# Kernel optimization log

Hardware: AMD Instinct MI355X
Metric: run time of the kernel (lower is better)

The kernel has to match this reference:

```python
import jax, jax.numpy as jnp
import numpy as np

EPS = 1e-5

def _ln(x, g, b):
    m = x.mean(-1, keepdims=True)
    v = ((x - m) ** 2).mean(-1, keepdims=True)
    return (x - m) * jax.lax.rsqrt(v + EPS) * g + b

def _glu(z):
    a, g = jnp.split(z, 2, axis=-1)
    return a * jax.nn.sigmoid(g)

def setup_inputs() -> dict:
    key = jax.random.key(0)
    ks = jax.random.split(key, 8)
    B, T, V, I, H = 64, 512, 32, 64, 64
    s = 0.02
    return {
        "x": jax.random.normal(ks[0], (B, T, V, I), dtype=jnp.float32),
        # weight GRN: (V*I) -> V
        "wg_W1": jax.random.normal(ks[1], (V * I, V), dtype=jnp.float32) * s,
        "wg_b1": jnp.zeros((V,), jnp.float32),
        "wg_W2": jax.random.normal(ks[2], (V, V), dtype=jnp.float32) * s,
        "wg_b2": jnp.zeros((V,), jnp.float32),
        "wg_Wg": jax.random.normal(ks[3], (V, 2 * V), dtype=jnp.float32) * s,
        "wg_bg": jnp.zeros((2 * V,), jnp.float32),
        "wg_Ws": jax.random.normal(ks[4], (V * I, V), dtype=jnp.float32) * s,
        "wg_bs": jnp.zeros((V,), jnp.float32),
        "wg_gamma": jnp.ones((V,), jnp.float32),
        "wg_beta": jnp.zeros((V,), jnp.float32),
        # per-variable GRNs, batched over V: I -> H (I == H, skip is identity)
        "v_W1": jax.random.normal(ks[5], (V, I, H), dtype=jnp.float32) * s,
        "v_b1": jnp.zeros((V, H), jnp.float32),
        "v_W2": jax.random.normal(ks[6], (V, H, H), dtype=jnp.float32) * s,
        "v_b2": jnp.zeros((V, H), jnp.float32),
        "v_Wg": jax.random.normal(ks[7], (V, H, 2 * H), dtype=jnp.float32) * s,
        "v_bg": jnp.zeros((V, 2 * H), jnp.float32),
        "v_gamma": jnp.ones((V, H), jnp.float32),
        "v_beta": jnp.zeros((V, H), jnp.float32),
    }

def reference(x, wg_W1, wg_b1, wg_W2, wg_b2, wg_Wg, wg_bg, wg_Ws, wg_bs,
              wg_gamma, wg_beta, v_W1, v_b1, v_W2, v_b2, v_Wg, v_bg,
              v_gamma, v_beta):
    B, T, V, I = x.shape
    # ---- variable-selection weights GRN on flattened input ----
    flat = x.reshape(B, T, V * I)                       # [B,T,V*I]
    skip = flat @ wg_Ws + wg_bs                          # [B,T,V] (proj skip: sizes differ)
    h = jax.nn.elu(flat @ wg_W1 + wg_b1)
    h = h @ wg_W2 + wg_b2
    w = _ln(skip + _glu(h @ wg_Wg + wg_bg), wg_gamma, wg_beta)
    w = jax.nn.softmax(w, axis=-1)                       # [B,T,V]
    # ---- per-variable GRNs, batched over V (skip = x since I == H) ----
    h = jax.nn.elu(jnp.einsum('btvi,vih->btvh', x, v_W1) + v_b1)
    h = jnp.einsum('btvh,vhk->btvk', h, v_W2) + v_b2
    g = jnp.einsum('btvh,vhk->btvk', h, v_Wg) + v_bg     # [B,T,V,2H]
    pv = _ln(x + _glu(g), v_gamma, v_beta)               # [B,T,V,H]
    # ---- softmax-weighted combination over variables ----
    return jnp.einsum('btv,btvh->bth', w, pv)            # [B,T,H]
```

## Files before the change

### kernel.cpp

```cpp
#include <hip/hip_runtime.h>

#define NT   32768
#define NV   32
#define DI   64
#define VI   2048

typedef __attribute__((ext_vector_type(8)))  short short8;
typedef __attribute__((ext_vector_type(16))) float floatx16;

#define MFMA32(a,b,c) __builtin_amdgcn_mfma_f32_32x32x16_bf16(a, b, c, 0, 0, 0)

#define WS_S      0
#define WS_WBUF   8388608
#define WS_WCOMBT 12582912
#define WS_WAV    12845056

static __device__ __forceinline__ unsigned short f2bf(float f) {
    union { float f; unsigned u; } v; v.f = f;
    unsigned r = v.u + 0x7FFFu + ((v.u >> 16) & 1u);
    return (unsigned short)(r >> 16);
}
static __device__ __forceinline__ unsigned pk2bf(float lo, float hi) {
    return (unsigned)f2bf(lo) | ((unsigned)f2bf(hi) << 16);
}
static __device__ __forceinline__ float elu1(float v) {
    return (v > 0.f) ? v : (__expf(v) - 1.f);
}

__global__ void k0_prep(const float* __restrict__ wg_W1, const float* __restrict__ wg_Ws,
                        const float* __restrict__ v_W1, const float* __restrict__ v_b1,
                        const float* __restrict__ v_W2, const float* __restrict__ v_b2,
                        const float* __restrict__ v_Wg, const float* __restrict__ v_bg,
                        unsigned short* __restrict__ WcombT, unsigned short* __restrict__ wAv) {
    int tid = blockIdx.x * blockDim.x + threadIdx.x;
    int stride = gridDim.x * blockDim.x;
    for (int i = tid; i < 64 * 2048; i += stride) {
        int n = i >> 11, k = i & 2047;
        float val = (n < 32) ? wg_Ws[k * 32 + n] : wg_W1[k * 32 + (n - 32)];
        WcombT[i] = f2bf(val);
    }
    for (int i = tid; i < 32 * 256 * 88; i += stride) {
        int v  = i / (256 * 88);
        int rm = i - v * (256 * 88);
        int r  = rm / 88, c = rm - r * 88;
        float val = 0.f;
        if (r < 64) {
            if (c < 64)       val = v_W1[(v * 64 + c) * 64 + r];
            else if (c == 64) val = v_b1[v * 64 + r];
        } else if (r < 128) {
            int m = r - 64;
            if (c < 64)       val = v_W2[(v * 64 + c) * 64 + m];
            else if (c == 64) val = v_b2[v * 64 + m];
        } else {
            int m = r - 128;
            if (c < 64)       val = v_Wg[(v * 64 + c) * 128 + m];
            else if (c == 64) val = v_bg[v * 128 + m];
        }
        wAv[i] = f2bf(val);
    }
}

__launch_bounds__(256, 4)
__global__ void k1_wgemm(const float* __restrict__ x, const unsigned short* __restrict__ WcombT,
                         const float* __restrict__ wg_bs, const float* __restrict__ wg_b1,
                         float* __restrict__ S) {
    __shared__ float Cbuf[4 * 64 * 33];
    int tid  = threadIdx.x;
    int wv   = tid >> 6;
    int lane = tid & 63;
    int l31  = lane & 31, s = lane >> 5;
    int tile = blockIdx.x;
    long tok = (long)tile * 32 + l31;

    const float*          xrow = x + tok * VI + wv * 512 + s * 8;
    const unsigned short* a0p  = WcombT + (l31)      * 2048 + wv * 512 + s * 8;
    const unsigned short* a1p  = WcombT + (l31 + 32) * 2048 + wv * 512 + s * 8;

    floatx16 acc0 = {}; floatx16 acc1 = {};
    #pragma unroll 4
    for (int ks = 0; ks < 32; ++ks) {
        int ko = ks * 16;
        short8 af0 = *(const short8*)(a0p + ko);
        short8 af1 = *(const short8*)(a1p + ko);
        float4 xa = *(const float4*)(xrow + ko);
        float4 xb = *(const float4*)(xrow + ko + 4);
        union { unsigned u[4]; short8 s8; } bp;
        bp.u[0] = pk2bf(xa.x, xa.y);
        bp.u[1] = pk2bf(xa.z, xa.w);
        bp.u[2] = pk2bf(xb.x, xb.y);
        bp.u[3] = pk2bf(xb.z, xb.w);
        acc0 = MFMA32(af0, bp.s8, acc0);
        acc1 = MFMA32(af1, bp.s8, acc1);
    }
    float* cb = Cbuf + wv * (64 * 33);
    #pragma unroll
    for (int reg = 0; reg < 16; ++reg) {
        int r0 = (reg & 3) + 8 * (reg >> 2) + 4 * s;
        cb[(r0)*33 + l31]      = acc0[reg];
        cb[(r0 + 32)*33 + l31] = acc1[reg];
    }
    __syncthreads();
    int n  = tid & 63;
    int tb = (tid >> 6) * 8;
    #pragma unroll
    for (int g = 0; g < 8; ++g) {
        int t = tb + g;
        float v = Cbuf[0*2112 + n*33 + t] + Cbuf[1*2112 + n*33 + t]
                + Cbuf[2*2112 + n*33 + t] + Cbuf[3*2112 + n*33 + t];
        if (n < 32) v += wg_bs[n];
        else        v = elu1(v + wg_b1[n - 32]);
        S[((long)tile * 32 + t) * 64 + n] = v;
    }
}

__launch_bounds__(256, 4)
__global__ void k2_token(const float* __restrict__ S,
                         const float* __restrict__ wg_W2, const float* __restrict__ wg_b2,
                         const float* __restrict__ wg_Wg, const float* __restrict__ wg_bg,
                         const float* __restrict__ wg_gamma, const float* __restrict__ wg_beta,
                         float* __restrict__ wout) {
    int tid = threadIdx.x;
    int wv = tid >> 6, lane = tid & 63;
    int l31 = lane & 31;
    long t = (long)blockIdx.x * 4 + wv;
    float sv = S[t * 64 + lane];
    float h2 = wg_b2[l31];
    #pragma unroll
    for (int k = 0; k < 32; ++k) {
        float h1e = __shfl(sv, 32 + k);
        h2 += h1e * wg_W2[k * 32 + l31];
    }
    float z = wg_bg[lane];
    #pragma unroll
    for (int k = 0; k < 32; ++k) {
        float hk = __shfl(h2, k);
        z += hk * wg_Wg[k * 64 + lane];
    }
    float za   = __shfl(z, l31);
    float zg   = __shfl(z, l31 + 32);
    float skip = __shfl(sv, l31);
    float y = skip + za / (1.f + __expf(-zg));
    float s1 = y;
    #pragma unroll
    for (int m = 1; m <= 16; m <<= 1) s1 += __shfl_xor(s1, m);
    float mean = s1 * (1.f / 32.f);
    float d = y - mean;
    float s2 = d * d;
    #pragma unroll
    for (int m = 1; m <= 16; m <<= 1) s2 += __shfl_xor(s2, m);
    float rinv  = rsqrtf(s2 * (1.f / 32.f) + 1e-5f);
    float logit = d * rinv * wg_gamma[l31] + wg_beta[l31];
    float mx = logit;
    #pragma unroll
    for (int m = 1; m <= 16; m <<= 1) mx = fmaxf(mx, __shfl_xor(mx, m));
    float e = __expf(logit - mx);
    float se = e;
    #pragma unroll
    for (int m = 1; m <= 16; m <<= 1) se += __shfl_xor(se, m);
    if (lane < 32) wout[t * 32 + lane] = e / se;
}

static __device__ __forceinline__ void tile_to_bfrags(const float* t16, int sh,
                                                      short8* f0, short8* f1) {
    unsigned P[8];
    #pragma unroll
    for (int i = 0; i < 8; ++i) P[i] = pk2bf(t16[2 * i], t16[2 * i + 1]);
    unsigned X[8];
    #pragma unroll
    for (int i = 0; i < 8; ++i) X[i] = (unsigned)__shfl_xor((int)P[i], 32);
    union { unsigned u[4]; short8 s8; } a, b;
    a.u[0] = sh ? X[2] : P[0];  a.u[1] = sh ? X[3] : P[1];
    a.u[2] = sh ? P[2] : X[0];  a.u[3] = sh ? P[3] : X[1];
    b.u[0] = sh ? X[6] : P[4];  b.u[1] = sh ? X[7] : P[5];
    b.u[2] = sh ? P[6] : X[4];  b.u[3] = sh ? P[7] : X[5];
    *f0 = a.s8; *f1 = b.s8;
}

__launch_bounds__(256, 2)
__global__ void k3_vgrn(const float* __restrict__ x, const unsigned short* __restrict__ wAv,
                        const float* __restrict__ v_gamma, const float* __restrict__ v_beta,
                        const float* __restrict__ wbuf, float* __restrict__ out) {
    __shared__ float xt[128 * 65];
    __shared__ __align__(16) unsigned short wA[256 * 88];
    __shared__ float gb[128];
    int tid  = threadIdx.x;
    int wv   = tid >> 6, lane = tid & 63;
    int l31  = lane & 31, s = lane >> 5;
    int tile = blockIdx.x >> 1;
    int vh   = blockIdx.x & 1;
    int tl   = wv * 32 + l31;
    long tokg = (long)tile * 128 + tl;

    float outacc[32];
    #pragma unroll
    for (int i = 0; i < 32; ++i) outacc[i] = 0.f;

    union { unsigned u[4]; short8 s8; } onef;
    onef.u[0] = (s == 0) ? 0x00003F80u : 0u;
    onef.u[1] = 0; onef.u[2] = 0; onef.u[3] = 0;

    const unsigned short* wArow = wA + l31 * 88 + s * 8;

    for (int it = 0; it < 16; ++it) {
        int vg = vh * 16 + it;
        __syncthreads();
        {
            const float* xsrc = x + ((long)tile * 128 * NV + vg) * DI;
            #pragma unroll
            for (int i2 = 0; i2 < 8; ++i2) {
                int idx = i2 * 256 + tid;
                int row = idx >> 4, c4 = (idx & 15) * 4;
                float4 val = *(const float4*)(xsrc + (long)row * VI + c4);
                float* dst = xt + row * 65 + c4;
                dst[0] = val.x; dst[1] = val.y; dst[2] = val.z; dst[3] = val.w;
            }
        }
        {
            const uint4* wsrc = (const uint4*)(wAv + (long)vg * 256 * 88);
            uint4* wdst = (uint4*)wA;
            #pragma unroll
            for (int i2 = 0; i2 < 11; ++i2) {
                int c = i2 * 256 + tid;
                wdst[c] = wsrc[c];
            }
        }
        if (tid < 128) {
            int h = tid >> 1;
            gb[tid] = (tid & 1) ? v_beta[vg * 64 + h] : v_gamma[vg * 64 + h];
        }
        __syncthreads();

        short8 xb[4];
        const float* xr = xt + tl * 65 + s * 8;
        #pragma unroll
        for (int ks = 0; ks < 4; ++ks) {
            const float* p = xr + ks * 16;
            union { unsigned u[4]; short8 s8; } bp;
            bp.u[0] = pk2bf(p[0], p[1]);
            bp.u[1] = pk2bf(p[2], p[3]);
            bp.u[2] = pk2bf(p[4], p[5]);
            bp.u[3] = pk2bf(p[6], p[7]);
            xb[ks] = bp.s8;
        }
        floatx16 h1a0 = {}, h1a1 = {};
        #pragma unroll
        for (int ks = 0; ks < 5; ++ks) {
            short8 b = (ks < 4) ? xb[ks] : onef.s8;
            h1a0 = MFMA32(*(const short8*)(wArow + (0)   * 88 + ks * 16), b, h1a0);
            h1a1 = MFMA32(*(const short8*)(wArow + (32)  * 88 + ks * 16), b, h1a1);
        }
        short8 h1b[4];
        {
            float t16[16];
            #pragma unroll
            for (int r = 0; r < 16; ++r) t16[r] = elu1(h1a0[r]);
            tile_to_bfrags(t16, s, &h1b[0], &h1b[1]);
            #pragma unroll
            for (int r = 0; r < 16; ++r) t16[r] = elu1(h1a1[r]);
            tile_to_bfrags(t16, s, &h1b[2], &h1b[3]);
        }
        floatx16 h2a0 = {}, h2a1 = {};
        #pragma unroll
        for (int ks = 0; ks < 5; ++ks) {
            short8 b = (ks < 4) ? h1b[ks] : onef.s8;
            h2a0 = MFMA32(*(const short8*)(wArow + (64)  * 88 + ks * 16), b, h2a0);
            h2a1 = MFMA32(*(const short8*)(wArow + (96)  * 88 + ks * 16), b, h2a1);
        }
        short8 h2b[4];
        {
            float t16[16];
            #pragma unroll
            for (int r = 0; r < 16; ++r) t16[r] = h2a0[r];
            tile_to_bfrags(t16, s, &h2b[0], &h2b[1]);
            #pragma unroll
            for (int r = 0; r < 16; ++r) t16[r] = h2a1[r];
            tile_to_bfrags(t16, s, &h2b[2], &h2b[3]);
        }
        floatx16 g0 = {}, g1 = {}, g2 = {}, g3 = {};
        #pragma unroll
        for (int ks = 0; ks < 5; ++ks) {
            short8 b = (ks < 4) ? h2b[ks] : onef.s8;
            g0 = MFMA32(*(const short8*)(wArow + (128) * 88 + ks * 16), b, g0);
            g1 = MFMA32(*(const short8*)(wArow + (160) * 88 + ks * 16), b, g1);
            g2 = MFMA32(*(const short8*)(wArow + (192) * 88 + ks * 16), b, g2);
            g3 = MFMA32(*(const short8*)(wArow + (224) * 88 + ks * 16), b, g3);
        }
        float y[32];
        #pragma unroll
        for (int r = 0; r < 16; ++r) {
            int hr = (r & 3) + 8 * (r >> 2) + 4 * s;
            float glu0 = g0[r] / (1.f + __expf(-g2[r]));
            float glu1 = g1[r] / (1.f + __expf(-g3[r]));
            y[r]      = xt[tl * 65 + hr]      + glu0;
            y[16 + r] = xt[tl * 65 + 32 + hr] + glu1;
        }
        float s1 = 0.f;
        #pragma unroll
        for (int i = 0; i < 32; ++i) s1 += y[i];
        s1 += __shfl_xor(s1, 32);
        float mean = s1 * (1.f / 64.f);
        float s2 = 0.f;
        #pragma unroll
        for (int i = 0; i < 32; ++i) { float d = y[i] - mean; s2 += d * d; }
        s2 += __shfl_xor(s2, 32);
        float rinv = rsqrtf(s2 * (1.f / 64.f) + 1e-5f);
        float wvv = wbuf[tokg * 32 + vg];
        #pragma unroll
        for (int r = 0; r < 16; ++r) {
            int hr = (r & 3) + 8 * (r >> 2) + 4 * s;
            float pv0 = (y[r]      - mean) * rinv * gb[2*hr]        + gb[2*hr + 1];
            float pv1 = (y[16 + r] - mean) * rinv * gb[2*(hr+32)]   + gb[2*(hr+32) + 1];
            outacc[r]      += wvv * pv0;
            outacc[16 + r] += wvv * pv1;
        }
    }
    #pragma unroll
    for (int r = 0; r < 16; ++r) {
        int hr = (r & 3) + 8 * (r >> 2) + 4 * s;
        atomicAdd(out + tokg * 64 + hr,      outacc[r]);
        atomicAdd(out + tokg * 64 + 32 + hr, outacc[16 + r]);
    }
}

extern "C" void kernel_launch(void* const* d_in, const int* in_sizes, int n_in,
                              void* d_out, int out_size, void* d_ws, size_t ws_size,
                              hipStream_t stream) {
    const float* x        = (const float*)d_in[0];
    const float* wg_W1    = (const float*)d_in[1];
    const float* wg_b1    = (const float*)d_in[2];
    const float* wg_W2    = (const float*)d_in[3];
    const float* wg_b2    = (const float*)d_in[4];
    const float* wg_Wg    = (const float*)d_in[5];
    const float* wg_bg    = (const float*)d_in[6];
    const float* wg_Ws    = (const float*)d_in[7];
    const float* wg_bs    = (const float*)d_in[8];
    const float* wg_gamma = (const float*)d_in[9];
    const float* wg_beta  = (const float*)d_in[10];
    const float* v_W1     = (const float*)d_in[11];
    const float* v_b1     = (const float*)d_in[12];
    const float* v_W2     = (const float*)d_in[13];
    const float* v_b2     = (const float*)d_in[14];
    const float* v_Wg     = (const float*)d_in[15];
    const float* v_bg     = (const float*)d_in[16];
    const float* v_gamma  = (const float*)d_in[17];
    const float* v_beta   = (const float*)d_in[18];
    (void)in_sizes; (void)n_in; (void)ws_size;

    char* ws = (char*)d_ws;
    float* S               = (float*)(ws + WS_S);
    float* wbuf            = (float*)(ws + WS_WBUF);
    unsigned short* WcombT = (unsigned short*)(ws + WS_WCOMBT);
    unsigned short* wAv    = (unsigned short*)(ws + WS_WAV);
    float* out             = (float*)d_out;

    hipMemsetAsync(d_out, 0, (size_t)out_size * sizeof(float), stream);
    k0_prep<<<512, 256, 0, stream>>>(wg_W1, wg_Ws, v_W1, v_b1, v_W2, v_b2, v_Wg, v_bg,
                                     WcombT, wAv);
    k1_wgemm<<<1024, 256, 0, stream>>>(x, WcombT, wg_bs, wg_b1, S);
    k2_token<<<8192, 256, 0, stream>>>(S, wg_W2, wg_b2, wg_Wg, wg_bg, wg_gamma, wg_beta, wbuf);
    k3_vgrn<<<512, 256, 0, stream>>>(x, wAv, v_gamma, v_beta, wbuf, out);
}
```

Before: 675.2 us.

## Fold W2 into gate weights and restructure per-variable GRN kernel

Since there is no nonlinearity between the second linear layer and the gate projection, the prep kernel now precomputes W2·Wg (plus the folded biases) for both the weight GRN and the per-variable GRNs. This removes one matmul stage per token in k2 and one MFMA stage in k3. k3 also stages x in shared memory as bf16, reuses those bf16 fragments via cross-lane shuffles for the residual, shrinks LDS so three blocks fit per CU, and splits variables into 4 groups of 8 over 1024 blocks, which doubles the number of atomic adds to the output. The folded product is computed in fp32 and then rounded to bf16, and the residual now uses bf16 x instead of fp32, which slightly changes numerics.

```diff
diff --git a/kernel.cpp b/kernel.cpp
--- a/kernel.cpp
+++ b/kernel.cpp
@@ -14,6 +14,8 @@
 #define WS_WBUF   8388608
 #define WS_WCOMBT 12582912
 #define WS_WAV    12845056
+#define WS_WC2    13926400
+#define WS_BC2    13934592
 
 static __device__ __forceinline__ unsigned short f2bf(float f) {
     union { float f; unsigned u; } v; v.f = f;
@@ -26,37 +28,68 @@
 static __device__ __forceinline__ float elu1(float v) {
     return (v > 0.f) ? v : (__expf(v) - 1.f);
 }
+static __device__ __forceinline__ float bflo(unsigned v) {
+    union { unsigned u; float f; } t; t.u = v << 16; return t.f;
+}
+static __device__ __forceinline__ float bfhi(unsigned v) {
+    union { unsigned u; float f; } t; t.u = v & 0xFFFF0000u; return t.f;
+}
 
 __global__ void k0_prep(const float* __restrict__ wg_W1, const float* __restrict__ wg_Ws,
+                        const float* __restrict__ wg_W2, const float* __restrict__ wg_b2,
+                        const float* __restrict__ wg_Wg, const float* __restrict__ wg_bg,
                         const float* __restrict__ v_W1, const float* __restrict__ v_b1,
                         const float* __restrict__ v_W2, const float* __restrict__ v_b2,
                         const float* __restrict__ v_Wg, const float* __restrict__ v_bg,
-                        unsigned short* __restrict__ WcombT, unsigned short* __restrict__ wAv) {
+                        unsigned short* __restrict__ WcombT, unsigned short* __restrict__ wAv,
+                        float* __restrict__ Wc2, float* __restrict__ bc2) {
     int tid = blockIdx.x * blockDim.x + threadIdx.x;
-    int stride = gridDim.x * blockDim.x;
-    for (int i = tid; i < 64 * 2048; i += stride) {
+    int np  = gridDim.x * blockDim.x;
+    for (int i = tid; i < 64 * 2048; i += np) {
         int n = i >> 11, k = i & 2047;
         float val = (n < 32) ? wg_Ws[k * 32 + n] : wg_W1[k * 32 + (n - 32)];
         WcombT[i] = f2bf(val);
     }
-    for (int i = tid; i < 32 * 256 * 88; i += stride) {
-        int v  = i / (256 * 88);
-        int rm = i - v * (256 * 88);
-        int r  = rm / 88, c = rm - r * 88;
+    for (int i = tid; i < 32 * 64 * 88; i += np) {
+        int v  = i / (64 * 88);
+        int rm = i - v * (64 * 88);
+        int h  = rm / 88, c = rm - h * 88;
         float val = 0.f;
-        if (r < 64) {
-            if (c < 64)       val = v_W1[(v * 64 + c) * 64 + r];
-            else if (c == 64) val = v_b1[v * 64 + r];
-        } else if (r < 128) {
-            int m = r - 64;
-            if (c < 64)       val = v_W2[(v * 64 + c) * 64 + m];
-            else if (c == 64) val = v_b2[v * 64 + m];
+        if (c < 64)       val = v_W1[(v * 64 + c) * 64 + h];
+        else if (c == 64) val = v_b1[v * 64 + h];
+        wAv[v * 16896 + h * 88 + c] = f2bf(val);
+    }
+    for (int i = tid; i < 32 * 128 * 88; i += np) {
+        int v  = i / (128 * 88);
+        int rm = i - v * (128 * 88);
+        int n  = rm / 88, c = rm - n * 88;
+        float acc = 0.f;
+        if (c < 64) {
+            #pragma unroll 8
+            for (int k = 0; k < 64; ++k)
+                acc += v_W2[(v * 64 + c) * 64 + k] * v_Wg[(v * 64 + k) * 128 + n];
+        } else if (c == 64) {
+            #pragma unroll 8
+            for (int k = 0; k < 64; ++k)
+                acc += v_b2[v * 64 + k] * v_Wg[(v * 64 + k) * 128 + n];
+            acc += v_bg[v * 128 + n];
+        }
+        wAv[v * 16896 + (64 + n) * 88 + c] = f2bf(acc);
+    }
+    for (int i = tid; i < 32 * 64 + 64; i += np) {
+        if (i < 2048) {
+            int j = i >> 6, n = i & 63;
+            float acc = 0.f;
+            #pragma unroll 8
+            for (int k = 0; k < 32; ++k) acc += wg_W2[j * 32 + k] * wg_Wg[k * 64 + n];
+            Wc2[i] = acc;
         } else {
-            int m = r - 128;
-            if (c < 64)       val = v_Wg[(v * 64 + c) * 128 + m];
-            else if (c == 64) val = v_bg[v * 128 + m];
-        }
-        wAv[i] = f2bf(val);
+            int n = i - 2048;
+            float acc = 0.f;
+            #pragma unroll 8
+            for (int k = 0; k < 32; ++k) acc += wg_b2[k] * wg_Wg[k * 64 + n];
+            bc2[n] = acc + wg_bg[n];
+        }
     }
 }
 
@@ -115,8 +148,7 @@
 
 __launch_bounds__(256, 4)
 __global__ void k2_token(const float* __restrict__ S,
-                         const float* __restrict__ wg_W2, const float* __restrict__ wg_b2,
-                         const float* __restrict__ wg_Wg, const float* __restrict__ wg_bg,
+                         const float* __restrict__ Wc2, const float* __restrict__ bc2,
                          const float* __restrict__ wg_gamma, const float* __restrict__ wg_beta,
                          float* __restrict__ wout) {
     int tid = threadIdx.x;
@@ -124,17 +156,11 @@
     int l31 = lane & 31;
     long t = (long)blockIdx.x * 4 + wv;
     float sv = S[t * 64 + lane];
-    float h2 = wg_b2[l31];
+    float z = bc2[lane];
     #pragma unroll
     for (int k = 0; k < 32; ++k) {
-        float h1e = __shfl(sv, 32 + k);
-        h2 += h1e * wg_W2[k * 32 + l31];
-    }
-    float z = wg_bg[lane];
-    #pragma unroll
-    for (int k = 0; k < 32; ++k) {
-        float hk = __shfl(h2, k);
-        z += hk * wg_Wg[k * 64 + lane];
+        float hk = __shfl(sv, 32 + k);
+        z += hk * Wc2[k * 64 + lane];
     }
     float za   = __shfl(z, l31);
     float zg   = __shfl(z, l31 + 32);
@@ -176,20 +202,20 @@
     *f0 = a.s8; *f1 = b.s8;
 }
 
-__launch_bounds__(256, 2)
+__launch_bounds__(256, 3)
 __global__ void k3_vgrn(const float* __restrict__ x, const unsigned short* __restrict__ wAv,
                         const float* __restrict__ v_gamma, const float* __restrict__ v_beta,
                         const float* __restrict__ wbuf, float* __restrict__ out) {
-    __shared__ float xt[128 * 65];
-    __shared__ __align__(16) unsigned short wA[256 * 88];
+    __shared__ __align__(16) unsigned short wA[192 * 88];
+    __shared__ __align__(16) unsigned short xt[128 * 72];
     __shared__ float gb[128];
     int tid  = threadIdx.x;
     int wv   = tid >> 6, lane = tid & 63;
     int l31  = lane & 31, s = lane >> 5;
-    int tile = blockIdx.x >> 1;
-    int vh   = blockIdx.x & 1;
+    int vg   = blockIdx.x & 3;
+    int tb   = blockIdx.x >> 2;
     int tl   = wv * 32 + l31;
-    long tokg = (long)tile * 128 + tl;
+    long tokg = (long)tb * 128 + tl;
 
     float outacc[32];
     #pragma unroll
@@ -200,54 +226,46 @@
     onef.u[1] = 0; onef.u[2] = 0; onef.u[3] = 0;
 
     const unsigned short* wArow = wA + l31 * 88 + s * 8;
-
-    for (int it = 0; it < 16; ++it) {
-        int vg = vh * 16 + it;
+    int srow = tid >> 1, shalf = tid & 1;
+
+    for (int j8 = 0; j8 < 8; ++j8) {
+        int v = vg * 8 + j8;
         __syncthreads();
         {
-            const float* xsrc = x + ((long)tile * 128 * NV + vg) * DI;
+            const uint4* src = (const uint4*)(wAv + (long)v * 16896);
+            uint4* dst = (uint4*)wA;
+            for (int c = tid; c < 2112; c += 256) dst[c] = src[c];
+        }
+        {
+            const float* xs = x + ((long)tb * 128 + srow) * VI + v * 64 + shalf * 32;
+            unsigned short* xd = xt + srow * 72 + shalf * 32;
             #pragma unroll
-            for (int i2 = 0; i2 < 8; ++i2) {
-                int idx = i2 * 256 + tid;
-                int row = idx >> 4, c4 = (idx & 15) * 4;
-                float4 val = *(const float4*)(xsrc + (long)row * VI + c4);
-                float* dst = xt + row * 65 + c4;
-                dst[0] = val.x; dst[1] = val.y; dst[2] = val.z; dst[3] = val.w;
-            }
-        }
-        {
-            const uint4* wsrc = (const uint4*)(wAv + (long)vg * 256 * 88);
-            uint4* wdst = (uint4*)wA;
-            #pragma unroll
-            for (int i2 = 0; i2 < 11; ++i2) {
-                int c = i2 * 256 + tid;
-                wdst[c] = wsrc[c];
+            for (int q = 0; q < 4; ++q) {
+                float4 a = ((const float4*)xs)[2 * q];
+                float4 b = ((const float4*)xs)[2 * q + 1];
+                uint4 w;
+                w.x = pk2bf(a.x, a.y); w.y = pk2bf(a.z, a.w);
+                w.z = pk2bf(b.x, b.y); w.w = pk2bf(b.z, b.w);
+                ((uint4*)xd)[q] = w;
             }
         }
         if (tid < 128) {
             int h = tid >> 1;
-            gb[tid] = (tid & 1) ? v_beta[vg * 64 + h] : v_gamma[vg * 64 + h];
+            gb[tid] = (tid & 1) ? v_beta[v * 64 + h] : v_gamma[v * 64 + h];
         }
         __syncthreads();
 
-        short8 xb[4];
-        const float* xr = xt + tl * 65 + s * 8;
-        #pragma unroll
-        for (int ks = 0; ks < 4; ++ks) {
-            const float* p = xr + ks * 16;
-            union { unsigned u[4]; short8 s8; } bp;
-            bp.u[0] = pk2bf(p[0], p[1]);
-            bp.u[1] = pk2bf(p[2], p[3]);
-            bp.u[2] = pk2bf(p[4], p[5]);
-            bp.u[3] = pk2bf(p[6], p[7]);
-            xb[ks] = bp.s8;
-        }
+        union { short8 s8; unsigned u[4]; } xb[4];
+        #pragma unroll
+        for (int ks = 0; ks < 4; ++ks)
+            xb[ks].s8 = *(const short8*)(xt + tl * 72 + ks * 16 + s * 8);
+
         floatx16 h1a0 = {}, h1a1 = {};
         #pragma unroll
         for (int ks = 0; ks < 5; ++ks) {
-            short8 b = (ks < 4) ? xb[ks] : onef.s8;
-            h1a0 = MFMA32(*(const short8*)(wArow + (0)   * 88 + ks * 16), b, h1a0);
-            h1a1 = MFMA32(*(const short8*)(wArow + (32)  * 88 + ks * 16), b, h1a1);
+            short8 b = (ks < 4) ? xb[ks].s8 : onef.s8;
+            h1a0 = MFMA32(*(const short8*)(wArow + 0    + ks * 16), b, h1a0);
+            h1a1 = MFMA32(*(const short8*)(wArow + 2816 + ks * 16), b, h1a1);
         }
         short8 h1b[4];
         {
@@ -259,40 +277,38 @@
             for (int r = 0; r < 16; ++r) t16[r] = elu1(h1a1[r]);
             tile_to_bfrags(t16, s, &h1b[2], &h1b[3]);
         }
-        floatx16 h2a0 = {}, h2a1 = {};
+        floatx16 g0 = {}, g1 = {}, g2 = {}, g3 = {};
         #pragma unroll
         for (int ks = 0; ks < 5; ++ks) {
             short8 b = (ks < 4) ? h1b[ks] : onef.s8;
-            h2a0 = MFMA32(*(const short8*)(wArow + (64)  * 88 + ks * 16), b, h2a0);
-            h2a1 = MFMA32(*(const short8*)(wArow + (96)  * 88 + ks * 16), b, h2a1);
-        }
-        short8 h2b[4];
-        {
-            float t16[16];
+            g0 = MFMA32(*(const short8*)(wArow + 2 * 2816 + ks * 16), b, g0);
+            g1 = MFMA32(*(const short8*)(wArow + 3 * 2816 + ks * 16), b, g1);
+            g2 = MFMA32(*(const short8*)(wArow + 4 * 2816 + ks * 16), b, g2);
+            g3 = MFMA32(*(const short8*)(wArow + 5 * 2816 + ks * 16), b, g3);
+        }
+        unsigned ownu[4][2], Xu[4][2];
+        #pragma unroll
+        for (int kk = 0; kk < 4; ++kk) {
             #pragma unroll
-            for (int r = 0; r < 16; ++r) t16[r] = h2a0[r];
-            tile_to_bfrags(t16, s, &h2b[0], &h2b[1]);
-            #pragma unroll
-            for (int r = 0; r < 16; ++r) t16[r] = h2a1[r];
-            tile_to_bfrags(t16, s, &h2b[2], &h2b[3]);
-        }
-        floatx16 g0 = {}, g1 = {}, g2 = {}, g3 = {};
-        #pragma unroll
-        for (int ks = 0; ks < 5; ++ks) {
-            short8 b = (ks < 4) ? h2b[ks] : onef.s8;
-            g0 = MFMA32(*(const short8*)(wArow + (128) * 88 + ks * 16), b, g0);
-            g1 = MFMA32(*(const short8*)(wArow + (160) * 88 + ks * 16), b, g1);
-            g2 = MFMA32(*(const short8*)(wArow + (192) * 88 + ks * 16), b, g2);
-            g3 = MFMA32(*(const short8*)(wArow + (224) * 88 + ks * 16), b, g3);
+            for (int d = 0; d < 2; ++d) {
+                ownu[kk][d] = s ? xb[kk].u[2 + d] : xb[kk].u[d];
+                unsigned R  = s ? xb[kk].u[d]     : xb[kk].u[2 + d];
+                Xu[kk][d]   = (unsigned)__shfl_xor((int)R, 32);
+            }
         }
         float y[32];
         #pragma unroll
         for (int r = 0; r < 16; ++r) {
-            int hr = (r & 3) + 8 * (r >> 2) + 4 * s;
-            float glu0 = g0[r] / (1.f + __expf(-g2[r]));
-            float glu1 = g1[r] / (1.f + __expf(-g3[r]));
-            y[r]      = xt[tl * 65 + hr]      + glu0;
-            y[16 + r] = xt[tl * 65 + 32 + hr] + glu1;
+            int a = r >> 2, b_ = r & 3, d = b_ >> 1, kk = a >> 1;
+            bool odd = (a & 1);
+            unsigned v0 = odd ? (s ? ownu[kk][d]     : Xu[kk][d])
+                              : (s ? Xu[kk][d]       : ownu[kk][d]);
+            unsigned v1 = odd ? (s ? ownu[2+kk][d]   : Xu[2+kk][d])
+                              : (s ? Xu[2+kk][d]     : ownu[2+kk][d]);
+            float sk0 = (b_ & 1) ? bfhi(v0) : bflo(v0);
+            float sk1 = (b_ & 1) ? bfhi(v1) : bflo(v1);
+            y[r]      = sk0 + g0[r] / (1.f + __expf(-g2[r]));
+            y[16 + r] = sk1 + g1[r] / (1.f + __expf(-g3[r]));
         }
         float s1 = 0.f;
         #pragma unroll
@@ -304,12 +320,12 @@
         for (int i = 0; i < 32; ++i) { float d = y[i] - mean; s2 += d * d; }
         s2 += __shfl_xor(s2, 32);
         float rinv = rsqrtf(s2 * (1.f / 64.f) + 1e-5f);
-        float wvv = wbuf[tokg * 32 + vg];
+        float wvv = wbuf[tokg * 32 + v];
         #pragma unroll
         for (int r = 0; r < 16; ++r) {
             int hr = (r & 3) + 8 * (r >> 2) + 4 * s;
-            float pv0 = (y[r]      - mean) * rinv * gb[2*hr]        + gb[2*hr + 1];
-            float pv1 = (y[16 + r] - mean) * rinv * gb[2*(hr+32)]   + gb[2*(hr+32) + 1];
+            float pv0 = (y[r]      - mean) * rinv * gb[2*hr]      + gb[2*hr + 1];
+            float pv1 = (y[16 + r] - mean) * rinv * gb[2*(hr+32)] + gb[2*(hr+32) + 1];
             outacc[r]      += wvv * pv0;
             outacc[16 + r] += wvv * pv1;
         }
@@ -351,12 +367,15 @@
     float* wbuf            = (float*)(ws + WS_WBUF);
     unsigned short* WcombT = (unsigned short*)(ws + WS_WCOMBT);
     unsigned short* wAv    = (unsigned short*)(ws + WS_WAV);
+    float* Wc2             = (float*)(ws + WS_WC2);
+    float* bc2             = (float*)(ws + WS_BC2);
     float* out             = (float*)d_out;
 
     hipMemsetAsync(d_out, 0, (size_t)out_size * sizeof(float), stream);
-    k0_prep<<<512, 256, 0, stream>>>(wg_W1, wg_Ws, v_W1, v_b1, v_W2, v_b2, v_Wg, v_bg,
-                                     WcombT, wAv);
+    k0_prep<<<512, 256, 0, stream>>>(wg_W1, wg_Ws, wg_W2, wg_b2, wg_Wg, wg_bg,
+                                     v_W1, v_b1, v_W2, v_b2, v_Wg, v_bg,
+                                     WcombT, wAv, Wc2, bc2);
     k1_wgemm<<<1024, 256, 0, stream>>>(x, WcombT, wg_bs, wg_b1, S);
-    k2_token<<<8192, 256, 0, stream>>>(S, wg_W2, wg_b2, wg_Wg, wg_bg, wg_gamma, wg_beta, wbuf);
-    k3_vgrn<<<512, 256, 0, stream>>>(x, wAv, v_gamma, v_beta, wbuf, out);
-}
+    k2_token<<<8192, 256, 0, stream>>>(S, Wc2, bc2, wg_gamma, wg_beta, wbuf);
+    k3_vgrn<<<1024, 256, 0, stream>>>(x, wAv, v_gamma, v_beta, wbuf, out);
+}
```

Result: slower. 774.5 us (+14.7%).
